# Kernel tuning notes

Hardware: AMD Instinct MI355X
Metric: run time of the kernel (lower is better)

Reference implementation:

```python
import jax, jax.numpy as jnp
import numpy as np

DIM = 1024
HEADS = 16
HEAD_DIM = DIM // HEADS
SCALE = HEAD_DIM ** -0.5


def setup_inputs() -> dict:
    key = jax.random.key(0)
    k1, k2, k3, k4 = jax.random.split(key, 4)
    x = jax.random.normal(k1, (4, 2048, DIM), dtype=jnp.float32)
    # nn.Linear weights stored as [out, in]; qkv_bias=False so no proj_in bias
    w_qkv = jax.random.normal(k2, (3 * DIM, DIM), dtype=jnp.float32) * (DIM ** -0.5)
    w_out = jax.random.normal(k3, (DIM, DIM), dtype=jnp.float32) * (DIM ** -0.5)
    b_out = jax.random.normal(k4, (DIM,), dtype=jnp.float32) * 0.01
    return {"x": x, "w_qkv": w_qkv, "w_out": w_out, "b_out": b_out}


def reference(x, w_qkv, w_out, b_out):
    bs, ns, _ = x.shape
    qkv = jnp.einsum("bsd,ed->bse", x, w_qkv)              # [b, s, 3*dim]
    qkv = qkv.reshape(bs, ns, 3, HEADS, HEAD_DIM)
    qkv = jnp.transpose(qkv, (2, 0, 3, 1, 4))               # [3, b, h, s, hd]
    q, k, v = qkv[0], qkv[1], qkv[2]
    attn = jnp.einsum("bhqd,bhkd->bhqk", q, k) * SCALE      # [b, h, s, s]
    attn = jax.nn.softmax(attn, axis=-1)
    out = jnp.einsum("bhqk,bhkd->bhqd", attn, v)            # [b, h, s, hd]
    out = jnp.transpose(out, (0, 2, 1, 3)).reshape(bs, ns, HEADS * HEAD_DIM)
    return jnp.einsum("bsd,ed->bse", out, w_out) + b_out
```

## Files before the change

kernel.cpp:

```cpp
#include <hip/hip_runtime.h>

#define DIM 1024
#define SEQ 2048

typedef unsigned short ushort_t;
typedef unsigned int u32;
typedef __attribute__((ext_vector_type(8))) short short8;
typedef __attribute__((ext_vector_type(8))) unsigned short ushort8;
typedef __attribute__((ext_vector_type(4))) float f32x4;
typedef __attribute__((ext_vector_type(16))) float f32x16;

__device__ __forceinline__ ushort_t f2bf(float x) {
    u32 u = __float_as_uint(x);
    u32 r = (u + 0x7fffu + ((u >> 16) & 1u)) >> 16;
    return (ushort_t)r;
}

__device__ __forceinline__ u32 cvtpk(float lo, float hi) {
    u32 r;
    asm("v_cvt_pk_bf16_f32 %0, %1, %2" : "=v"(r) : "v"(lo), "v"(hi));
    return r;
}

__device__ __forceinline__ float max3f(float a, float b, float c) {
    float d;
    asm("v_max3_f32 %0, %1, %2, %3" : "=v"(d) : "v"(a), "v"(b), "v"(c));
    return d;
}

__device__ __forceinline__ void gload16(const void* g, void* l) {
    __builtin_amdgcn_global_load_lds(
        (const __attribute__((address_space(1))) u32*)g,
        (__attribute__((address_space(3))) u32*)l, 16, 0, 0);
}

__device__ __forceinline__ int swz8(int row, int col) {
    return row * 64 + ((((col >> 3) ^ (row & 7)) << 3) | (col & 7));
}

__global__ __launch_bounds__(256) void cvt_bf16(const float* __restrict__ in,
                                                ushort_t* __restrict__ out, int n8) {
    for (int i = blockIdx.x * blockDim.x + threadIdx.x; i < n8; i += gridDim.x * blockDim.x) {
        const float4 a = ((const float4*)in)[2 * i];
        const float4 b = ((const float4*)in)[2 * i + 1];
        ushort8 o;
        o[0] = f2bf(a.x); o[1] = f2bf(a.y); o[2] = f2bf(a.z); o[3] = f2bf(a.w);
        o[4] = f2bf(b.x); o[5] = f2bf(b.y); o[6] = f2bf(b.z); o[7] = f2bf(b.w);
        ((ushort8*)out)[i] = o;
    }
}

template <int EPI>
__global__ __launch_bounds__(256) void gemm_bt(const ushort_t* __restrict__ A,
                                               const ushort_t* __restrict__ B,
                                               const float* __restrict__ bias,
                                               ushort_t* __restrict__ outb,
                                               ushort_t* __restrict__ voutb,
                                               float* __restrict__ outf) {
    __shared__ __align__(16) ushort_t As[128 * 64];
    __shared__ __align__(16) ushort_t Bs[128 * 64];
    const int t = threadIdx.x;
    const int m0 = blockIdx.y * 128, n0 = blockIdx.x * 128;
    const int w = t >> 6, lane = t & 63, k15 = lane & 15, g = lane >> 4;
    const int wm = (w >> 1) * 64, wn = (w & 1) * 64;
    const int srow = t >> 3, scol = (t & 7) * 8;

    f32x4 acc[4][4] = {};

    for (int k0 = 0; k0 < 1024; k0 += 64) {
        __syncthreads();
        #pragma unroll
        for (int i = 0; i < 4; ++i) {
            gload16(&A[(size_t)(m0 + i * 32 + srow) * 1024 + k0 + scol],
                    ((char*)As) + i * 4096 + t * 16);
            gload16(&B[(size_t)(n0 + i * 32 + srow) * 1024 + k0 + scol],
                    ((char*)Bs) + i * 4096 + t * 16);
        }
        __syncthreads();
        #pragma unroll
        for (int ks = 0; ks < 2; ++ks) {
            short8 af[4], bf[4];
            #pragma unroll
            for (int i = 0; i < 4; ++i) {
                af[i] = *(const short8*)&As[(wm + i * 16 + k15) * 64 + ks * 32 + g * 8];
                bf[i] = *(const short8*)&Bs[(wn + i * 16 + k15) * 64 + ks * 32 + g * 8];
            }
            #pragma unroll
            for (int mi = 0; mi < 4; ++mi)
                #pragma unroll
                for (int ni = 0; ni < 4; ++ni)
                    acc[mi][ni] = __builtin_amdgcn_mfma_f32_16x16x32_bf16(
                        af[mi], bf[ni], acc[mi][ni], 0, 0, 0);
        }
    }

    if (EPI == 0) {
        #pragma unroll
        for (int mi = 0; mi < 4; ++mi) {
            const int mbase = m0 + wm + mi * 16 + g * 4;
            const int b = mbase >> 11, s0 = mbase & 2047;
            #pragma unroll
            for (int ni = 0; ni < 4; ++ni) {
                const int e = n0 + wn + ni * 16 + k15;
                const int qi = e >> 10, h = (e >> 6) & 15, hd = e & 63;
                const int bh = b * 16 + h;
                if (qi == 2) {
                    const u32 lo = cvtpk(acc[mi][ni][0], acc[mi][ni][1]);
                    const u32 hi = cvtpk(acc[mi][ni][2], acc[mi][ni][3]);
                    *(uint2*)&voutb[((size_t)bh * 64 + hd) * SEQ + s0] = make_uint2(lo, hi);
                } else {
                    const float scl = (qi == 0) ? 0.180336880f : 1.0f;
                    #pragma unroll
                    for (int r = 0; r < 4; ++r)
                        outb[((size_t)(qi * 64 + bh) * SEQ + s0 + r) * 64 + hd] =
                            f2bf(acc[mi][ni][r] * scl);
                }
            }
        }
    } else {
        #pragma unroll
        for (int mi = 0; mi < 4; ++mi) {
            #pragma unroll
            for (int r = 0; r < 4; ++r) {
                const size_t m = m0 + wm + mi * 16 + g * 4 + r;
                #pragma unroll
                for (int ni = 0; ni < 4; ++ni) {
                    const int e = n0 + wn + ni * 16 + k15;
                    outf[m * 1024 + e] = acc[mi][ni][r] + bias[e];
                }
            }
        }
    }
}

__global__ __launch_bounds__(256, 4) void attn_mfma(const ushort_t* __restrict__ qk,
                                                    const ushort_t* __restrict__ vt,
                                                    ushort_t* __restrict__ aout) {
    __shared__ __align__(16) ushort_t Ks[2][64 * 64];
    __shared__ __align__(16) ushort_t Vs[2][64 * 64];

    const int t = threadIdx.x, w = t >> 6, lane = t & 63;
    const int l31 = lane & 31, hi = lane >> 5;

    const int bid = blockIdx.x + (blockIdx.y << 4);
    const int j   = bid >> 3;
    const int bh  = ((bid & 7) << 3) + (j >> 4);
    const int q0  = (j & 15) * 128;

    const ushort_t* Qp = qk + (size_t)bh * SEQ * 64;
    const ushort_t* Kp = qk + (size_t)(64 + bh) * SEQ * 64;
    const ushort_t* Vp = vt + (size_t)bh * 64 * SEQ;
    const int wq = q0 + w * 32 + l31;

    const int srow = t >> 3;
    const int scb8 = ((t & 7) ^ (srow & 7)) * 8;

    const ushort_t* kpA = Kp + (size_t)srow * 64 + scb8;
    const ushort_t* vpA = Vp + (size_t)srow * SEQ + scb8;

    short8 qf[4];
    #pragma unroll
    for (int kc = 0; kc < 4; ++kc)
        qf[kc] = *(const short8*)&Qp[(size_t)wq * 64 + kc * 16 + hi * 8];

    gload16(kpA,            ((char*)Ks) + t * 16);
    gload16(kpA + 32 * 64,  ((char*)Ks) + 4096 + t * 16);
    gload16(vpA,            ((char*)Vs) + t * 16);
    gload16(vpA + 32 * SEQ, ((char*)Vs) + 4096 + t * 16);
    kpA += 64 * 64; vpA += 64;
    __syncthreads();

    f32x16 o2[2] = {};
    float mi = -1e30f, li = 0.f;
    int cur = 0;

    for (int kt = 0; kt < SEQ / 64; ++kt) {
        if (kt + 1 < SEQ / 64) {
            char* dstK = ((char*)Ks) + (cur ^ 1) * 8192 + t * 16;
            char* dstV = ((char*)Vs) + (cur ^ 1) * 8192 + t * 16;
            gload16(kpA,            dstK);
            gload16(kpA + 32 * 64,  dstK + 4096);
            gload16(vpA,            dstV);
            gload16(vpA + 32 * SEQ, dstV + 4096);
            kpA += 64 * 64; vpA += 64;
        }

        f32x16 s32[2] = {};
        __builtin_amdgcn_s_setprio(1);
        #pragma unroll
        for (int kt2 = 0; kt2 < 2; ++kt2) {
            #pragma unroll
            for (int kc = 0; kc < 4; ++kc) {
                const short8 kf = *(const short8*)&Ks[cur][swz8(kt2 * 32 + l31, kc * 16 + hi * 8)];
                s32[kt2] = __builtin_amdgcn_mfma_f32_32x32x16_bf16(
                    kf, qf[kc], s32[kt2], 0, 0, 0);
            }
        }
        __builtin_amdgcn_s_setprio(0);

        {
            const f32x16 a = s32[0], b = s32[1];
            float w0 = max3f(a[0], a[1], a[2]);
            float w1 = max3f(a[3], a[4], a[5]);
            float w2 = max3f(a[6], a[7], a[8]);
            float w3 = max3f(a[9], a[10], a[11]);
            float w4 = max3f(a[12], a[13], a[14]);
            float w5 = max3f(a[15], b[0], b[1]);
            float w6 = max3f(b[2], b[3], b[4]);
            float w7 = max3f(b[5], b[6], b[7]);
            float w8 = max3f(b[8], b[9], b[10]);
            float w9 = max3f(b[11], b[12], b[13]);
            float wA = fmaxf(b[14], b[15]);
            float u0 = max3f(w0, w1, w2);
            float u1 = max3f(w3, w4, w5);
            float u2 = max3f(w6, w7, w8);
            float u3 = fmaxf(w9, wA);
            float vm = fmaxf(max3f(u0, u1, u2), u3);
            vm = fmaxf(vm, __shfl_xor(vm, 32));
            if (__any(vm > mi + 8.0f)) {
                const float mnew = fmaxf(mi, vm);
                const float c = __builtin_amdgcn_exp2f(mi - mnew);
                mi = mnew;
                li *= c;
                #pragma unroll
                for (int dt = 0; dt < 2; ++dt)
                    #pragma unroll
                    for (int r = 0; r < 16; ++r)
                        o2[dt][r] *= c;
            }
        }
        {
            float t0 = 0.f, t1 = 0.f, t2 = 0.f, t3 = 0.f;
            #pragma unroll
            for (int kt2 = 0; kt2 < 2; ++kt2) {
                #pragma unroll
                for (int r = 0; r < 16; r += 4) {
                    const float e0 = __builtin_amdgcn_exp2f(s32[kt2][r + 0] - mi);
                    const float e1 = __builtin_amdgcn_exp2f(s32[kt2][r + 1] - mi);
                    const float e2 = __builtin_amdgcn_exp2f(s32[kt2][r + 2] - mi);
                    const float e3 = __builtin_amdgcn_exp2f(s32[kt2][r + 3] - mi);
                    s32[kt2][r + 0] = e0; s32[kt2][r + 1] = e1;
                    s32[kt2][r + 2] = e2; s32[kt2][r + 3] = e3;
                    t0 += e0; t1 += e1; t2 += e2; t3 += e3;
                }
            }
            float rs = (t0 + t1) + (t2 + t3);
            rs += __shfl_xor(rs, 32);
            li += rs;
        }

        uint4 pb[4];
        #pragma unroll
        for (int ks2 = 0; ks2 < 4; ++ks2) {
            const int r0 = (ks2 & 1) * 8;
            const int sv = ks2 >> 1;
            u32 pA = cvtpk(s32[sv][r0 + 0], s32[sv][r0 + 1]);
            u32 pB = cvtpk(s32[sv][r0 + 2], s32[sv][r0 + 3]);
            u32 pC = cvtpk(s32[sv][r0 + 4], s32[sv][r0 + 5]);
            u32 pD = cvtpk(s32[sv][r0 + 6], s32[sv][r0 + 7]);
            asm volatile("v_permlane32_swap_b32 %0, %1" : "+v"(pA), "+v"(pC));
            asm volatile("v_permlane32_swap_b32 %0, %1" : "+v"(pB), "+v"(pD));
            pb[ks2] = make_uint4(pA, pB, pC, pD);
        }

        __builtin_amdgcn_s_setprio(1);
        #pragma unroll
        for (int dt = 0; dt < 2; ++dt) {
            #pragma unroll
            for (int ks2 = 0; ks2 < 4; ++ks2) {
                const short8 vf = *(const short8*)&Vs[cur][swz8(dt * 32 + l31, ks2 * 16 + hi * 8)];
                o2[dt] = __builtin_amdgcn_mfma_f32_32x32x16_bf16(
                    vf, *(const short8*)&pb[ks2], o2[dt], 0, 0, 0);
            }
        }
        __builtin_amdgcn_s_setprio(0);

        __syncthreads();
        cur ^= 1;
    }

    const int b = bh >> 4, h = bh & 15;
    const float inv = 1.0f / li;
    const size_t base = ((size_t)b * SEQ + wq) * DIM + h * 64;
    #pragma unroll
    for (int dt = 0; dt < 2; ++dt) {
        #pragma unroll
        for (int rq = 0; rq < 4; ++rq) {
            const u32 lo = cvtpk(o2[dt][4 * rq + 0] * inv, o2[dt][4 * rq + 1] * inv);
            const u32 hg = cvtpk(o2[dt][4 * rq + 2] * inv, o2[dt][4 * rq + 3] * inv);
            *(uint2*)&aout[base + dt * 32 + rq * 8 + hi * 4] = make_uint2(lo, hg);
        }
    }
}

extern "C" void kernel_launch(void* const* d_in, const int* in_sizes, int n_in,
                              void* d_out, int out_size, void* d_ws, size_t ws_size,
                              hipStream_t stream) {
    const float* x     = (const float*)d_in[0];
    const float* w_qkv = (const float*)d_in[1];
    const float* w_out = (const float*)d_in[2];
    const float* b_out = (const float*)d_in[3];
    float* out = (float*)d_out;

    char* ws = (char*)d_ws;
    ushort_t* xb    = (ushort_t*)ws;
    ushort_t* wqkvb = (ushort_t*)(ws + (size_t)16 * 1024 * 1024);
    ushort_t* woutb = (ushort_t*)(ws + (size_t)22 * 1024 * 1024);
    ushort_t* qkb   = (ushort_t*)(ws + (size_t)24 * 1024 * 1024);
    ushort_t* vtb   = (ushort_t*)(ws + (size_t)56 * 1024 * 1024);
    ushort_t* aob   = (ushort_t*)(ws + (size_t)72 * 1024 * 1024);

    cvt_bf16<<<1024, 256, 0, stream>>>(x,     xb,    8192 * 1024 / 8);
    cvt_bf16<<<512,  256, 0, stream>>>(w_qkv, wqkvb, 3072 * 1024 / 8);
    cvt_bf16<<<256,  256, 0, stream>>>(w_out, woutb, 1024 * 1024 / 8);

    gemm_bt<0><<<dim3(24, 64), 256, 0, stream>>>(xb, wqkvb, nullptr, qkb, vtb, nullptr);
    attn_mfma<<<dim3(16, 64), 256, 0, stream>>>(qkb, vtb, aob);
    gemm_bt<1><<<dim3(8, 64), 256, 0, stream>>>(aob, woutb, b_out, nullptr, nullptr, out);
}
```

Baseline: 220.2 us.

## Software-pipeline attention: overlap next QK^T tile with softmax/PV, triple-buffer K/V

```diff
diff --git a/kernel.cpp b/kernel.cpp
--- a/kernel.cpp
+++ b/kernel.cpp
@@ -133,27 +133,141 @@
     }
 }
 
-__global__ __launch_bounds__(256, 4) void attn_mfma(const ushort_t* __restrict__ qk,
+struct AttnState {
+    f32x16 o2[2];
+    float mi, li;
+};
+
+__device__ __forceinline__ void qk_tile(f32x16 (&sb)[2], const ushort_t* Ks,
+                                        int off, const short8 (&qf)[4],
+                                        int l31, int hi) {
+    sb[0] = (f32x16){}; sb[1] = (f32x16){};
+    __builtin_amdgcn_s_setprio(1);
+    #pragma unroll
+    for (int kt2 = 0; kt2 < 2; ++kt2) {
+        #pragma unroll
+        for (int kc = 0; kc < 4; ++kc) {
+            const short8 kf = *(const short8*)&Ks[off * 4096 +
+                swz8(kt2 * 32 + l31, kc * 16 + hi * 8)];
+            sb[kt2] = __builtin_amdgcn_mfma_f32_32x32x16_bf16(
+                kf, qf[kc], sb[kt2], 0, 0, 0);
+        }
+    }
+    __builtin_amdgcn_s_setprio(0);
+}
+
+__device__ __forceinline__ void pipe_step(
+    int t, f32x16 (&sa)[2], f32x16 (&sb)[2], AttnState& st,
+    const ushort_t*& kpA, const ushort_t*& vpA,
+    ushort_t* Ks, ushort_t* Vs, int oPV, int oQK, int oST,
+    int tid, const short8 (&qf)[4], int l31, int hi) {
+    if (t + 2 < 32) {
+        gload16(kpA, ((char*)Ks) + oST * 8192 + tid * 16);
+        gload16(vpA, ((char*)Vs) + oST * 8192 + tid * 16);
+        kpA += 4096; vpA += 64;
+    }
+    if (t + 1 < 32) qk_tile(sb, Ks, oQK, qf, l31, hi);
+
+    {
+        const f32x16 a = sa[0], b = sa[1];
+        float w0 = max3f(a[0], a[1], a[2]);
+        float w1 = max3f(a[3], a[4], a[5]);
+        float w2 = max3f(a[6], a[7], a[8]);
+        float w3 = max3f(a[9], a[10], a[11]);
+        float w4 = max3f(a[12], a[13], a[14]);
+        float w5 = max3f(a[15], b[0], b[1]);
+        float w6 = max3f(b[2], b[3], b[4]);
+        float w7 = max3f(b[5], b[6], b[7]);
+        float w8 = max3f(b[8], b[9], b[10]);
+        float w9 = max3f(b[11], b[12], b[13]);
+        float wA = fmaxf(b[14], b[15]);
+        float u0 = max3f(w0, w1, w2);
+        float u1 = max3f(w3, w4, w5);
+        float u2 = max3f(w6, w7, w8);
+        float u3 = fmaxf(w9, wA);
+        float vm = fmaxf(max3f(u0, u1, u2), u3);
+        vm = fmaxf(vm, __shfl_xor(vm, 32));
+        if (__any(vm > st.mi + 8.0f)) {
+            const float mnew = fmaxf(st.mi, vm);
+            const float c = __builtin_amdgcn_exp2f(st.mi - mnew);
+            st.mi = mnew;
+            st.li *= c;
+            #pragma unroll
+            for (int dt = 0; dt < 2; ++dt)
+                #pragma unroll
+                for (int r = 0; r < 16; ++r)
+                    st.o2[dt][r] *= c;
+        }
+        float t0 = 0.f, t1 = 0.f, t2 = 0.f, t3 = 0.f;
+        #pragma unroll
+        for (int kt2 = 0; kt2 < 2; ++kt2) {
+            #pragma unroll
+            for (int r = 0; r < 16; r += 4) {
+                const float e0 = __builtin_amdgcn_exp2f(sa[kt2][r + 0] - st.mi);
+                const float e1 = __builtin_amdgcn_exp2f(sa[kt2][r + 1] - st.mi);
+                const float e2 = __builtin_amdgcn_exp2f(sa[kt2][r + 2] - st.mi);
+                const float e3 = __builtin_amdgcn_exp2f(sa[kt2][r + 3] - st.mi);
+                sa[kt2][r + 0] = e0; sa[kt2][r + 1] = e1;
+                sa[kt2][r + 2] = e2; sa[kt2][r + 3] = e3;
+                t0 += e0; t1 += e1; t2 += e2; t3 += e3;
+            }
+        }
+        float rs = (t0 + t1) + (t2 + t3);
+        rs += __shfl_xor(rs, 32);
+        st.li += rs;
+    }
+
+    uint4 pb[4];
+    #pragma unroll
+    for (int ks2 = 0; ks2 < 4; ++ks2) {
+        const int r0 = (ks2 & 1) * 8;
+        const int sv = ks2 >> 1;
+        u32 pA = cvtpk(sa[sv][r0 + 0], sa[sv][r0 + 1]);
+        u32 pB = cvtpk(sa[sv][r0 + 2], sa[sv][r0 + 3]);
+        u32 pC = cvtpk(sa[sv][r0 + 4], sa[sv][r0 + 5]);
+        u32 pD = cvtpk(sa[sv][r0 + 6], sa[sv][r0 + 7]);
+        asm volatile("v_permlane32_swap_b32 %0, %1" : "+v"(pA), "+v"(pC));
+        asm volatile("v_permlane32_swap_b32 %0, %1" : "+v"(pB), "+v"(pD));
+        pb[ks2] = make_uint4(pA, pB, pC, pD);
+    }
+
+    __builtin_amdgcn_s_setprio(1);
+    #pragma unroll
+    for (int dt = 0; dt < 2; ++dt) {
+        #pragma unroll
+        for (int ks2 = 0; ks2 < 4; ++ks2) {
+            const short8 vf = *(const short8*)&Vs[oPV * 4096 +
+                swz8(dt * 32 + l31, ks2 * 16 + hi * 8)];
+            st.o2[dt] = __builtin_amdgcn_mfma_f32_32x32x16_bf16(
+                vf, *(const short8*)&pb[ks2], st.o2[dt], 0, 0, 0);
+        }
+    }
+    __builtin_amdgcn_s_setprio(0);
+
+    __syncthreads();
+}
+
+__global__ __launch_bounds__(512, 4) void attn_mfma(const ushort_t* __restrict__ qk,
                                                     const ushort_t* __restrict__ vt,
                                                     ushort_t* __restrict__ aout) {
-    __shared__ __align__(16) ushort_t Ks[2][64 * 64];
-    __shared__ __align__(16) ushort_t Vs[2][64 * 64];
-
-    const int t = threadIdx.x, w = t >> 6, lane = t & 63;
+    __shared__ __align__(16) ushort_t Ks[3 * 64 * 64];
+    __shared__ __align__(16) ushort_t Vs[3 * 64 * 64];
+
+    const int tid = threadIdx.x, w = tid >> 6, lane = tid & 63;
     const int l31 = lane & 31, hi = lane >> 5;
 
-    const int bid = blockIdx.x + (blockIdx.y << 4);
+    const int bid = blockIdx.x;
     const int j   = bid >> 3;
-    const int bh  = ((bid & 7) << 3) + (j >> 4);
-    const int q0  = (j & 15) * 128;
+    const int bh  = ((bid & 7) << 3) + (j >> 3);
+    const int q0  = (j & 7) * 256;
 
     const ushort_t* Qp = qk + (size_t)bh * SEQ * 64;
     const ushort_t* Kp = qk + (size_t)(64 + bh) * SEQ * 64;
     const ushort_t* Vp = vt + (size_t)bh * 64 * SEQ;
     const int wq = q0 + w * 32 + l31;
 
-    const int srow = t >> 3;
-    const int scb8 = ((t & 7) ^ (srow & 7)) * 8;
+    const int srow = tid >> 3;
+    const int scb8 = ((tid & 7) ^ (srow & 7)) * 8;
 
     const ushort_t* kpA = Kp + (size_t)srow * 64 + scb8;
     const ushort_t* vpA = Vp + (size_t)srow * SEQ + scb8;
@@ -163,131 +277,39 @@
     for (int kc = 0; kc < 4; ++kc)
         qf[kc] = *(const short8*)&Qp[(size_t)wq * 64 + kc * 16 + hi * 8];
 
-    gload16(kpA,            ((char*)Ks) + t * 16);
-    gload16(kpA + 32 * 64,  ((char*)Ks) + 4096 + t * 16);
-    gload16(vpA,            ((char*)Vs) + t * 16);
-    gload16(vpA + 32 * SEQ, ((char*)Vs) + 4096 + t * 16);
-    kpA += 64 * 64; vpA += 64;
+    gload16(kpA,        ((char*)Ks) + tid * 16);
+    gload16(vpA,        ((char*)Vs) + tid * 16);
+    gload16(kpA + 4096, ((char*)Ks) + 8192 + tid * 16);
+    gload16(vpA + 64,   ((char*)Vs) + 8192 + tid * 16);
+    kpA += 2 * 4096; vpA += 2 * 64;
     __syncthreads();
 
-    f32x16 o2[2] = {};
-    float mi = -1e30f, li = 0.f;
-    int cur = 0;
-
-    for (int kt = 0; kt < SEQ / 64; ++kt) {
-        if (kt + 1 < SEQ / 64) {
-            char* dstK = ((char*)Ks) + (cur ^ 1) * 8192 + t * 16;
-            char* dstV = ((char*)Vs) + (cur ^ 1) * 8192 + t * 16;
-            gload16(kpA,            dstK);
-            gload16(kpA + 32 * 64,  dstK + 4096);
-            gload16(vpA,            dstV);
-            gload16(vpA + 32 * SEQ, dstV + 4096);
-            kpA += 64 * 64; vpA += 64;
-        }
-
-        f32x16 s32[2] = {};
-        __builtin_amdgcn_s_setprio(1);
-        #pragma unroll
-        for (int kt2 = 0; kt2 < 2; ++kt2) {
-            #pragma unroll
-            for (int kc = 0; kc < 4; ++kc) {
-                const short8 kf = *(const short8*)&Ks[cur][swz8(kt2 * 32 + l31, kc * 16 + hi * 8)];
-                s32[kt2] = __builtin_amdgcn_mfma_f32_32x32x16_bf16(
-                    kf, qf[kc], s32[kt2], 0, 0, 0);
-            }
-        }
-        __builtin_amdgcn_s_setprio(0);
-
-        {
-            const f32x16 a = s32[0], b = s32[1];
-            float w0 = max3f(a[0], a[1], a[2]);
-            float w1 = max3f(a[3], a[4], a[5]);
-            float w2 = max3f(a[6], a[7], a[8]);
-            float w3 = max3f(a[9], a[10], a[11]);
-            float w4 = max3f(a[12], a[13], a[14]);
-            float w5 = max3f(a[15], b[0], b[1]);
-            float w6 = max3f(b[2], b[3], b[4]);
-            float w7 = max3f(b[5], b[6], b[7]);
-            float w8 = max3f(b[8], b[9], b[10]);
-            float w9 = max3f(b[11], b[12], b[13]);
-            float wA = fmaxf(b[14], b[15]);
-            float u0 = max3f(w0, w1, w2);
-            float u1 = max3f(w3, w4, w5);
-            float u2 = max3f(w6, w7, w8);
-            float u3 = fmaxf(w9, wA);
-            float vm = fmaxf(max3f(u0, u1, u2), u3);
-            vm = fmaxf(vm, __shfl_xor(vm, 32));
-            if (__any(vm > mi + 8.0f)) {
-                const float mnew = fmaxf(mi, vm);
-                const float c = __builtin_amdgcn_exp2f(mi - mnew);
-                mi = mnew;
-                li *= c;
-                #pragma unroll
-                for (int dt = 0; dt < 2; ++dt)
-                    #pragma unroll
-                    for (int r = 0; r < 16; ++r)
-                        o2[dt][r] *= c;
-            }
-        }
-        {
-            float t0 = 0.f, t1 = 0.f, t2 = 0.f, t3 = 0.f;
-            #pragma unroll
-            for (int kt2 = 0; kt2 < 2; ++kt2) {
-                #pragma unroll
-                for (int r = 0; r < 16; r += 4) {
-                    const float e0 = __builtin_amdgcn_exp2f(s32[kt2][r + 0] - mi);
-                    const float e1 = __builtin_amdgcn_exp2f(s32[kt2][r + 1] - mi);
-                    const float e2 = __builtin_amdgcn_exp2f(s32[kt2][r + 2] - mi);
-                    const float e3 = __builtin_amdgcn_exp2f(s32[kt2][r + 3] - mi);
-                    s32[kt2][r + 0] = e0; s32[kt2][r + 1] = e1;
-                    s32[kt2][r + 2] = e2; s32[kt2][r + 3] = e3;
-                    t0 += e0; t1 += e1; t2 += e2; t3 += e3;
-                }
-            }
-            float rs = (t0 + t1) + (t2 + t3);
-            rs += __shfl_xor(rs, 32);
-            li += rs;
-        }
-
-        uint4 pb[4];
-        #pragma unroll
-        for (int ks2 = 0; ks2 < 4; ++ks2) {
-            const int r0 = (ks2 & 1) * 8;
-            const int sv = ks2 >> 1;
-            u32 pA = cvtpk(s32[sv][r0 + 0], s32[sv][r0 + 1]);
-            u32 pB = cvtpk(s32[sv][r0 + 2], s32[sv][r0 + 3]);
-            u32 pC = cvtpk(s32[sv][r0 + 4], s32[sv][r0 + 5]);
-            u32 pD = cvtpk(s32[sv][r0 + 6], s32[sv][r0 + 7]);
-            asm volatile("v_permlane32_swap_b32 %0, %1" : "+v"(pA), "+v"(pC));
-            asm volatile("v_permlane32_swap_b32 %0, %1" : "+v"(pB), "+v"(pD));
-            pb[ks2] = make_uint4(pA, pB, pC, pD);
-        }
-
-        __builtin_amdgcn_s_setprio(1);
-        #pragma unroll
-        for (int dt = 0; dt < 2; ++dt) {
-            #pragma unroll
-            for (int ks2 = 0; ks2 < 4; ++ks2) {
-                const short8 vf = *(const short8*)&Vs[cur][swz8(dt * 32 + l31, ks2 * 16 + hi * 8)];
-                o2[dt] = __builtin_amdgcn_mfma_f32_32x32x16_bf16(
-                    vf, *(const short8*)&pb[ks2], o2[dt], 0, 0, 0);
-            }
-        }
-        __builtin_amdgcn_s_setprio(0);
-
-        __syncthreads();
-        cur ^= 1;
+    AttnState st;
+    st.o2[0] = (f32x16){}; st.o2[1] = (f32x16){};
+    st.mi = -1e30f; st.li = 0.f;
+
+    f32x16 sX[2], sY[2];
+    qk_tile(sX, Ks, 0, qf, l31, hi);
+
+    int oPV = 0, oQK = 1, oST = 2;
+    for (int tt = 0; tt < 32; tt += 2) {
+        pipe_step(tt, sX, sY, st, kpA, vpA, Ks, Vs, oPV, oQK, oST,
+                  tid, qf, l31, hi);
+        { int tmp = oPV; oPV = oQK; oQK = oST; oST = tmp; }
+        pipe_step(tt + 1, sY, sX, st, kpA, vpA, Ks, Vs, oPV, oQK, oST,
+                  tid, qf, l31, hi);
+        { int tmp = oPV; oPV = oQK; oQK = oST; oST = tmp; }
     }
 
     const int b = bh >> 4, h = bh & 15;
-    const float inv = 1.0f / li;
+    const float inv = 1.0f / st.li;
     const size_t base = ((size_t)b * SEQ + wq) * DIM + h * 64;
     #pragma unroll
     for (int dt = 0; dt < 2; ++dt) {
         #pragma unroll
         for (int rq = 0; rq < 4; ++rq) {
-            const u32 lo = cvtpk(o2[dt][4 * rq + 0] * inv, o2[dt][4 * rq + 1] * inv);
-            const u32 hg = cvtpk(o2[dt][4 * rq + 2] * inv, o2[dt][4 * rq + 3] * inv);
+            const u32 lo = cvtpk(st.o2[dt][4 * rq + 0] * inv, st.o2[dt][4 * rq + 1] * inv);
+            const u32 hg = cvtpk(st.o2[dt][4 * rq + 2] * inv, st.o2[dt][4 * rq + 3] * inv);
             *(uint2*)&aout[base + dt * 32 + rq * 8 + hi * 4] = make_uint2(lo, hg);
         }
     }
@@ -315,6 +337,6 @@
     cvt_bf16<<<256,  256, 0, stream>>>(w_out, woutb, 1024 * 1024 / 8);
 
     gemm_bt<0><<<dim3(24, 64), 256, 0, stream>>>(xb, wqkvb, nullptr, qkb, vtb, nullptr);
-    attn_mfma<<<dim3(16, 64), 256, 0, stream>>>(qkb, vtb, aob);
+    attn_mfma<<<512, 512, 0, stream>>>(qkb, vtb, aob);
     gemm_bt<1><<<dim3(8, 64), 256, 0, stream>>>(aob, woutb, b_out, nullptr, nullptr, out);
 }
```

Result: slower. 280.1 us (+27.2%).
